# Performance work log

Hardware: AMD Instinct MI355X
Metric: run time of the kernel (lower is better)

## Reference

```python
import jax, jax.numpy as jnp
import numpy as np

N_NODES = 20000
N_EDGES = 320000
N_GRAPHS = 64
IN_FEAT = 64
HIDDEN = 256
GRID = 4
NUM_LAYERS = 4  # -> 3 Fourier message-passing layers
NEG_SLOPE = 0.01  # nn.LeakyReLU default


def setup_inputs() -> dict:
    key = jax.random.key(0)
    ks = jax.random.split(key, 8)
    h = jax.random.normal(ks[0], (N_NODES, IN_FEAT), dtype=jnp.float32)
    src = jax.random.randint(ks[1], (N_EDGES,), 0, N_NODES, dtype=jnp.int32)
    dst = jax.random.randint(ks[2], (N_EDGES,), 0, N_NODES, dtype=jnp.int32)
    graph_ids = jnp.sort(jax.random.randint(ks[3], (N_NODES,), 0, N_GRAPHS, dtype=jnp.int32))
    # KAN_polynomial(in_feat, hidden, degree=grid_feat), init randn/(sqrt(in)*sqrt(deg))
    W_line = jax.random.normal(ks[4], (HIDDEN, IN_FEAT, GRID + 1), dtype=jnp.float32) / (
        np.sqrt(IN_FEAT) * np.sqrt(GRID))
    # 3 NaiveFourierKANLayer coeffs [2, out, in, grid]
    fourier_coeffs = jax.random.normal(ks[5], (NUM_LAYERS - 1, 2, HIDDEN, HIDDEN, GRID),
                                       dtype=jnp.float32) / (np.sqrt(HIDDEN) * np.sqrt(GRID))
    # Readout KAN_polynomial(hidden, 1, degree=1, addbias=True)
    W_out = jax.random.normal(ks[6], (1, HIDDEN, 2), dtype=jnp.float32) / np.sqrt(HIDDEN)
    b_out = jnp.zeros((1, 1), dtype=jnp.float32)
    return {"h": h, "src": src, "dst": dst, "graph_ids": graph_ids,
            "W_line": W_line, "fourier_coeffs": fourier_coeffs,
            "W_out": W_out, "b_out": b_out}


def kan_polynomial(x, coeffs, bias=None):
    # x: [b, in], coeffs: [out, in, deg+1]
    deg = coeffs.shape[-1] - 1
    powers = jnp.stack([x ** i for i in range(deg + 1)], axis=-1)  # [b, in, deg+1]
    y = jnp.einsum('bid,oid->bo', powers, coeffs)
    if bias is not None:
        y = y + bias
    return y


def fourier_kan(x, coeffs):
    # x: [N, in], coeffs: [2, out, in, grid]
    grid = coeffs.shape[-1]
    k = jnp.arange(1, grid + 1, dtype=x.dtype)  # [grid]
    ang = x[:, :, None] * k  # [N, in, grid]
    y = jnp.einsum('nig,oig->no', jnp.cos(ang), coeffs[0])
    y = y + jnp.einsum('nig,oig->no', jnp.sin(ang), coeffs[1])
    return y


def reference(h, src, dst, graph_ids, W_line, fourier_coeffs, W_out, b_out):
    # kan_line
    h = kan_polynomial(h, W_line)  # [N, hidden]
    # message-passing Fourier KAN layers with residual + leaky_relu
    for l in range(NUM_LAYERS - 1):
        agg = jax.ops.segment_sum(h[src], dst, num_segments=N_NODES)  # copy_u + sum
        m = fourier_kan(agg, fourier_coeffs[l])
        h = jax.nn.leaky_relu(m + h, negative_slope=NEG_SLOPE)
    # avg pooling per graph
    sums = jax.ops.segment_sum(h, graph_ids, num_segments=N_GRAPHS)  # [G, hidden]
    counts = jax.ops.segment_sum(jnp.ones((N_NODES,), dtype=h.dtype), graph_ids,
                                 num_segments=N_GRAPHS)
    y = sums / jnp.maximum(counts, 1.0)[:, None]
    # Readout: KAN_polynomial(hidden, 1, degree=1) + sigmoid
    out = jax.nn.sigmoid(kan_polynomial(y, W_out, b_out))  # [G, 1]
    return out
```

## Files before the change

kernel.cpp:

```cpp
#include <hip/hip_runtime.h>
#include <math.h>

#define N_NODES   20000
#define N_PAD2    20096
#define N_EDGES   320000
#define N_GRAPHS  64
#define IN_FEAT   64
#define HIDDEN    256
#define GRID_F    4
#define NLAYERS   3
#define NEG_SLOPE 0.01f

#define KF 2048
#define KL4 256
#define NB_SCAN 79
#define NRG  157
#define NBLK (NRG * 4)
#define NLBLK 1256

typedef _Float16 f16x8 __attribute__((ext_vector_type(8)));
typedef _Float16 f16x2 __attribute__((ext_vector_type(2)));
typedef float    f32x4 __attribute__((ext_vector_type(4)));

__global__ void transpose_fourier_f16(const float* __restrict__ fc, _Float16* __restrict__ Bt) {
    int idx = blockIdx.x * 256 + threadIdx.x;
    int kk  = idx & 2047;
    int rest = idx >> 11;
    int o = rest & 255;
    int l = rest >> 8;
    int i = kk >> 3, f = kk & 7, g = f >> 1, t = f & 1;
    Bt[idx] = (_Float16)fc[(((size_t)(l * 2 + t) * HIDDEN + o) * HIDDEN + i) * GRID_F + g];
}

__global__ void transpose_line4(const float* __restrict__ wl, _Float16* __restrict__ Wth,
                                _Float16* __restrict__ Wtl) {
    int idx = blockIdx.x * 256 + threadIdx.x;
    int o = idx >> 8, kk = idx & 255;
    int i = kk >> 2, d = (kk & 3) + 1;
    float wv = wl[(o * IN_FEAT + i) * 5 + d];
    _Float16 h = (_Float16)wv;
    Wth[idx] = h;
    Wtl[idx] = (_Float16)(wv - (float)h);
}

__global__ void line_bias(const float* __restrict__ wl, float* __restrict__ biasv) {
    int o = threadIdx.x;
    float s = 0.f;
    for (int i = 0; i < IN_FEAT; ++i) s += wl[(o * IN_FEAT + i) * 5];
    biasv[o] = s;
}

__global__ void count_deg(const int* __restrict__ dst, int* __restrict__ counts) {
    int e = blockIdx.x * 256 + threadIdx.x;
    if (e < N_EDGES) atomicAdd(&counts[dst[e]], 1);
}

__global__ void block_sums(const int* __restrict__ counts, int* __restrict__ bsum) {
    int i = blockIdx.x * 256 + threadIdx.x;
    int v = (i < N_NODES) ? counts[i] : 0;
    #pragma unroll
    for (int o = 32; o > 0; o >>= 1) v += __shfl_down(v, o, 64);
    __shared__ int ws[4];
    if ((threadIdx.x & 63) == 0) ws[threadIdx.x >> 6] = v;
    __syncthreads();
    if (threadIdx.x == 0) bsum[blockIdx.x] = ws[0] + ws[1] + ws[2] + ws[3];
}

__global__ void scan_mid(const int* __restrict__ bsum, int* __restrict__ bofs,
                         int* __restrict__ row_start) {
    __shared__ int buf[128];
    int t = threadIdx.x;
    int v = (t < NB_SCAN) ? bsum[t] : 0;
    buf[t] = v;
    __syncthreads();
    for (int d = 1; d < 128; d <<= 1) {
        int x = (t >= d) ? buf[t - d] : 0;
        __syncthreads();
        buf[t] += x;
        __syncthreads();
    }
    if (t < NB_SCAN) bofs[t] = buf[t] - v;
    if (t == NB_SCAN - 1) row_start[N_NODES] = buf[t];
}

__global__ void scan_blocks(const int* __restrict__ counts, const int* __restrict__ bofs,
                            int* __restrict__ row_start) {
    int i = blockIdx.x * 256 + threadIdx.x;
    int val = (i < N_NODES) ? counts[i] : 0;
    int lane = threadIdx.x & 63, wid = threadIdx.x >> 6;
    int v = val;
    #pragma unroll
    for (int d = 1; d < 64; d <<= 1) {
        int t = __shfl_up(v, d, 64);
        if (lane >= d) v += t;
    }
    __shared__ int ws[4];
    if (lane == 63) ws[wid] = v;
    __syncthreads();
    int wofs = 0;
    for (int j = 0; j < wid; ++j) wofs += ws[j];
    if (i < N_NODES) row_start[i] = bofs[blockIdx.x] + wofs + v - val;
}

__global__ void fill_csr(const int* __restrict__ src, const int* __restrict__ dst,
                         const int* __restrict__ row_start, int* __restrict__ cursor,
                         int* __restrict__ ssrc) {
    int e = blockIdx.x * 256 + threadIdx.x;
    if (e < N_EDGES) {
        int d = dst[e];
        int pos = row_start[d] + atomicAdd(&cursor[d], 1);
        ssrc[pos] = src[e];
    }
}

__global__ __launch_bounds__(256)
void aggregate(const float* __restrict__ h, const int* __restrict__ row_start,
               const int* __restrict__ ssrc, unsigned* __restrict__ cs) {
    const int node = blockIdx.x * 4 + (threadIdx.x >> 6);
    const int lane = threadIdx.x & 63;
    const int b = row_start[node], e = row_start[node + 1];
    f32x4 a0 = {0.f, 0.f, 0.f, 0.f}, a1 = {0.f, 0.f, 0.f, 0.f};
    f32x4 a2 = {0.f, 0.f, 0.f, 0.f}, a3 = {0.f, 0.f, 0.f, 0.f};
    int j = b;
    for (; j + 3 < e; j += 4) {
        int s0 = ssrc[j], s1 = ssrc[j + 1], s2 = ssrc[j + 2], s3 = ssrc[j + 3];
        a0 += *(const f32x4*)&h[(size_t)s0 * HIDDEN + lane * 4];
        a1 += *(const f32x4*)&h[(size_t)s1 * HIDDEN + lane * 4];
        a2 += *(const f32x4*)&h[(size_t)s2 * HIDDEN + lane * 4];
        a3 += *(const f32x4*)&h[(size_t)s3 * HIDDEN + lane * 4];
    }
    for (; j < e; ++j) {
        int s0 = ssrc[j];
        a0 += *(const f32x4*)&h[(size_t)s0 * HIDDEN + lane * 4];
    }
    f32x4 v = (a0 + a1) + (a2 + a3);
    unsigned csv[4];
    #pragma unroll
    for (int k = 0; k < 4; ++k) {
        float r = v[k] * 0.15915494309189535f;
        r -= floorf(r);
        _Float16 ch = (_Float16)__builtin_amdgcn_cosf(r);
        _Float16 sh = (_Float16)__builtin_amdgcn_sinf(r);
        union { f16x2 z; unsigned u; } p;
        p.z = (f16x2){ch, sh};
        csv[k] = p.u;
    }
    *(uint4*)&cs[(size_t)node * HIDDEN + lane * 4] = make_uint4(csv[0], csv[1], csv[2], csv[3]);
}

__device__ __forceinline__ void makepow(float xa, float xb, f16x8& hi, f16x8& lo) {
    float p0 = xa, p1 = xa * xa;
    float p2 = p1 * xa, p3 = p1 * p1;
    float q0 = xb, q1 = xb * xb;
    float q2 = q1 * xb, q3 = q1 * q1;
    float pp[8] = {p0, p1, p2, p3, q0, q1, q2, q3};
    #pragma unroll
    for (int j = 0; j < 8; ++j) {
        _Float16 h = (_Float16)pp[j];
        hi[j] = h;
        lo[j] = (_Float16)(pp[j] - (float)h);
    }
}

__global__ __launch_bounds__(256)
void kan_line_mfma(const float* __restrict__ x, const _Float16* __restrict__ Wth,
                   const _Float16* __restrict__ Wtl, const float* __restrict__ biasv,
                   float* __restrict__ out) {
    __shared__ float    As[64][64];
    __shared__ _Float16 Bsh[64][136];
    __shared__ _Float16 Bsl[64][136];

    const int t = threadIdx.x;
    const int w = t >> 6, l = t & 63, ln = l & 15, quad = l >> 4;
    const int wr = w >> 1, wc = w & 1;

    const int g   = blockIdx.x;
    const int bid = (g & 7) * 157 + (g >> 3);
    const int Mbase = (bid >> 2) * 64;
    const int col0  = (bid & 3) * 64;

    #pragma unroll
    for (int r = 0; r < 4; ++r) {
        int idx = r * 256 + t;
        int row = idx >> 4, p = idx & 15;
        int grow = Mbase + row;
        if (grow > N_NODES - 1) grow = N_NODES - 1;
        f32x4 v = *(const f32x4*)&x[(size_t)grow * IN_FEAT + p * 4];
        *(f32x4*)&As[row][(p * 4) ^ ((row & 7) << 2)] = v;
    }
    const _Float16* WthB = Wth + (size_t)col0 * KL4;
    const _Float16* WtlB = Wtl + (size_t)col0 * KL4;
    #pragma unroll
    for (int r = 0; r < 4; ++r) {
        int idx = r * 256 + t;
        int c = idx >> 4, p = idx & 15;
        *(f16x8*)&Bsh[c][p * 8] = *(const f16x8*)&WthB[(size_t)c * KL4 + p * 8];
        *(f16x8*)&Bsl[c][p * 8] = *(const f16x8*)&WtlB[(size_t)c * KL4 + p * 8];
    }
    f16x8 pbh[4], pbl[4];
    #pragma unroll
    for (int r = 0; r < 4; ++r) {
        int idx = r * 256 + t;
        int c = idx >> 4, p = idx & 15;
        pbh[r] = *(const f16x8*)&WthB[(size_t)c * KL4 + 128 + p * 8];
        pbl[r] = *(const f16x8*)&WtlB[(size_t)c * KL4 + 128 + p * 8];
    }
    __syncthreads();

    f32x4 acc[2][2];
    #pragma unroll
    for (int rt = 0; rt < 2; ++rt)
        #pragma unroll
        for (int ct = 0; ct < 2; ++ct)
            acc[rt][ct] = (f32x4){0.f, 0.f, 0.f, 0.f};

    const int lr0 = wr * 32 + ln;
    const int xsw = (lr0 & 7) << 2;

    #pragma unroll
    for (int half = 0; half < 2; ++half) {
        #pragma unroll
        for (int kcl = 0; kcl < 4; ++kcl) {
            const int kc = half * 4 + kcl;
            const int f0 = kc * 8 + quad * 2;
            float x00 = As[lr0     ][f0 ^ xsw];
            float x01 = As[lr0     ][(f0 + 1) ^ xsw];
            float x10 = As[lr0 + 16][f0 ^ xsw];
            float x11 = As[lr0 + 16][(f0 + 1) ^ xsw];
            f16x8 ah0, al0, ah1, al1;
            makepow(x00, x01, ah0, al0);
            makepow(x10, x11, ah1, al1);
            #pragma unroll
            for (int ct = 0; ct < 2; ++ct) {
                const int bc = wc * 32 + ct * 16 + ln;
                f16x8 bh = *(const f16x8*)&Bsh[bc][kcl * 32 + quad * 8];
                f16x8 bl = *(const f16x8*)&Bsl[bc][kcl * 32 + quad * 8];
                acc[0][ct] = __builtin_amdgcn_mfma_f32_16x16x32_f16(ah0, bh, acc[0][ct], 0, 0, 0);
                acc[0][ct] = __builtin_amdgcn_mfma_f32_16x16x32_f16(al0, bh, acc[0][ct], 0, 0, 0);
                acc[0][ct] = __builtin_amdgcn_mfma_f32_16x16x32_f16(ah0, bl, acc[0][ct], 0, 0, 0);
                acc[1][ct] = __builtin_amdgcn_mfma_f32_16x16x32_f16(ah1, bh, acc[1][ct], 0, 0, 0);
                acc[1][ct] = __builtin_amdgcn_mfma_f32_16x16x32_f16(al1, bh, acc[1][ct], 0, 0, 0);
                acc[1][ct] = __builtin_amdgcn_mfma_f32_16x16x32_f16(ah1, bl, acc[1][ct], 0, 0, 0);
            }
        }
        if (half == 0) {
            __syncthreads();
            #pragma unroll
            for (int r = 0; r < 4; ++r) {
                int idx = r * 256 + t;
                int c = idx >> 4, p = idx & 15;
                *(f16x8*)&Bsh[c][p * 8] = pbh[r];
                *(f16x8*)&Bsl[c][p * 8] = pbl[r];
            }
            __syncthreads();
        }
    }

    #pragma unroll
    for (int rt = 0; rt < 2; ++rt) {
        const int row0 = Mbase + wr * 32 + rt * 16 + quad * 4;
        #pragma unroll
        for (int ct = 0; ct < 2; ++ct) {
            const int col = col0 + wc * 32 + ct * 16 + ln;
            const float bv = biasv[col];
            #pragma unroll
            for (int r = 0; r < 4; ++r) {
                const int row = row0 + r;
                if (row < N_NODES)
                    out[(size_t)row * HIDDEN + col] = acc[rt][ct][r] + bv;
            }
        }
    }
}

__device__ __forceinline__ f16x8 expand4(unsigned csu) {
    union { unsigned u; f16x2 z; } w; w.u = csu;
    f16x2 z1 = w.z;
    f16x2 cc = {z1[0], z1[0]};
    f16x2 ms = {(_Float16)(-z1[1]), z1[1]};
    f16x2 z2 = z1 * cc + (f16x2){z1[1], z1[0]} * ms;
    f16x2 z3 = z2 * cc + (f16x2){z2[1], z2[0]} * ms;
    f16x2 z4 = z3 * cc + (f16x2){z3[1], z3[0]} * ms;
    union { f16x8 v; f16x2 p[4]; } u;
    u.p[0] = z1; u.p[1] = z2; u.p[2] = z3; u.p[3] = z4;
    return u.v;
}

__global__ __launch_bounds__(256)
void fourier_mfma(const unsigned* __restrict__ cs, float* hio,
                  const _Float16* __restrict__ Bt) {
    __shared__ _Float16 Bs[2][64][140];
    __shared__ unsigned As[2][128][17];

    const int t    = threadIdx.x;
    const int w    = t >> 6;
    const int l    = t & 63;
    const int ln   = l & 15;
    const int quad = l >> 4;

    const int g   = blockIdx.x;
    const int xcd = g & 7, ii = g >> 3;
    const int bid = (xcd < 4 ? xcd * 79 : 316 + (xcd - 4) * 78) + ii;
    const int Mbase = (bid >> 2) * 128;
    const int col0  = (bid & 3) * 64;

    const int sc = t >> 4, sp = t & 15;
    const int sr = t >> 2, sq = t & 3;
    const _Float16* bg0 = Bt + (size_t)(col0 + sc) * KF + sp * 8;
    const _Float16* bg1 = bg0 + (size_t)16 * KF;
    const _Float16* bg2 = bg0 + (size_t)32 * KF;
    const _Float16* bg3 = bg0 + (size_t)48 * KF;
    const unsigned* ag0 = cs + (size_t)(Mbase + sr) * HIDDEN + sq * 4;
    const unsigned* ag1 = ag0 + (size_t)64 * HIDDEN;

    f32x4 acc[2][4];
    #pragma unroll
    for (int rt = 0; rt < 2; ++rt)
        #pragma unroll
        for (int ct = 0; ct < 4; ++ct)
            acc[rt][ct] = (f32x4){0.f, 0.f, 0.f, 0.f};

    f16x8 sb0, sb1, sb2, sb3;
    uint4 sa0, sa1;

    sb0 = *(const f16x8*)(bg0);
    sb1 = *(const f16x8*)(bg1);
    sb2 = *(const f16x8*)(bg2);
    sb3 = *(const f16x8*)(bg3);
    sa0 = *(const uint4*)(ag0);
    sa1 = *(const uint4*)(ag1);
    *(f16x8*)&Bs[0][sc     ][sp * 8] = sb0;
    *(f16x8*)&Bs[0][sc + 16][sp * 8] = sb1;
    *(f16x8*)&Bs[0][sc + 32][sp * 8] = sb2;
    *(f16x8*)&Bs[0][sc + 48][sp * 8] = sb3;
    As[0][sr     ][sq * 4 + 0] = sa0.x;
    As[0][sr     ][sq * 4 + 1] = sa0.y;
    As[0][sr     ][sq * 4 + 2] = sa0.z;
    As[0][sr     ][sq * 4 + 3] = sa0.w;
    As[0][sr + 64][sq * 4 + 0] = sa1.x;
    As[0][sr + 64][sq * 4 + 1] = sa1.y;
    As[0][sr + 64][sq * 4 + 2] = sa1.z;
    As[0][sr + 64][sq * 4 + 3] = sa1.w;
    __syncthreads();

    const int lr0 = w * 32 + ln;

    for (int kg = 0; kg < 16; ++kg) {
        const int b = kg & 1;
        if (kg < 15) {
            sb0 = *(const f16x8*)(bg0 + (kg + 1) * 128);
            sb1 = *(const f16x8*)(bg1 + (kg + 1) * 128);
            sb2 = *(const f16x8*)(bg2 + (kg + 1) * 128);
            sb3 = *(const f16x8*)(bg3 + (kg + 1) * 128);
            sa0 = *(const uint4*)(ag0 + (kg + 1) * 16);
            sa1 = *(const uint4*)(ag1 + (kg + 1) * 16);
        }
        #pragma unroll
        for (int kc = 0; kc < 4; ++kc) {
            unsigned cv0 = As[b][lr0     ][kc * 4 + quad];
            unsigned cv1 = As[b][lr0 + 16][kc * 4 + quad];
            f16x8 b0 = *(const f16x8*)&Bs[b][ln     ][kc * 32 + quad * 8];
            f16x8 b1 = *(const f16x8*)&Bs[b][ln + 16][kc * 32 + quad * 8];
            f16x8 b2 = *(const f16x8*)&Bs[b][ln + 32][kc * 32 + quad * 8];
            f16x8 b3 = *(const f16x8*)&Bs[b][ln + 48][kc * 32 + quad * 8];
            f16x8 a0 = expand4(cv0);
            f16x8 a1 = expand4(cv1);
            acc[0][0] = __builtin_amdgcn_mfma_f32_16x16x32_f16(a0, b0, acc[0][0], 0, 0, 0);
            acc[0][1] = __builtin_amdgcn_mfma_f32_16x16x32_f16(a0, b1, acc[0][1], 0, 0, 0);
            acc[0][2] = __builtin_amdgcn_mfma_f32_16x16x32_f16(a0, b2, acc[0][2], 0, 0, 0);
            acc[0][3] = __builtin_amdgcn_mfma_f32_16x16x32_f16(a0, b3, acc[0][3], 0, 0, 0);
            acc[1][0] = __builtin_amdgcn_mfma_f32_16x16x32_f16(a1, b0, acc[1][0], 0, 0, 0);
            acc[1][1] = __builtin_amdgcn_mfma_f32_16x16x32_f16(a1, b1, acc[1][1], 0, 0, 0);
            acc[1][2] = __builtin_amdgcn_mfma_f32_16x16x32_f16(a1, b2, acc[1][2], 0, 0, 0);
            acc[1][3] = __builtin_amdgcn_mfma_f32_16x16x32_f16(a1, b3, acc[1][3], 0, 0, 0);
        }
        if (kg < 15) {
            const int nb = b ^ 1;
            *(f16x8*)&Bs[nb][sc     ][sp * 8] = sb0;
            *(f16x8*)&Bs[nb][sc + 16][sp * 8] = sb1;
            *(f16x8*)&Bs[nb][sc + 32][sp * 8] = sb2;
            *(f16x8*)&Bs[nb][sc + 48][sp * 8] = sb3;
            As[nb][sr     ][sq * 4 + 0] = sa0.x;
            As[nb][sr     ][sq * 4 + 1] = sa0.y;
            As[nb][sr     ][sq * 4 + 2] = sa0.z;
            As[nb][sr     ][sq * 4 + 3] = sa0.w;
            As[nb][sr + 64][sq * 4 + 0] = sa1.x;
            As[nb][sr + 64][sq * 4 + 1] = sa1.y;
            As[nb][sr + 64][sq * 4 + 2] = sa1.z;
            As[nb][sr + 64][sq * 4 + 3] = sa1.w;
        }
        __syncthreads();
    }

    #pragma unroll
    for (int rt = 0; rt < 2; ++rt) {
        const int row0 = Mbase + w * 32 + rt * 16 + quad * 4;
        #pragma unroll
        for (int ct = 0; ct < 4; ++ct) {
            const int col = col0 + ct * 16 + ln;
            #pragma unroll
            for (int r = 0; r < 4; ++r) {
                const int row = row0 + r;
                if (row < N_NODES) {
                    float v = acc[rt][ct][r] + hio[(size_t)row * HIDDEN + col];
                    v = v > 0.f ? v : NEG_SLOPE * v;
                    hio[(size_t)row * HIDDEN + col] = v;
                }
            }
        }
    }
}

__global__ void graph_bounds(const int* __restrict__ gid, int* __restrict__ gstart) {
    int g = threadIdx.x;
    if (g < N_GRAPHS) {
        int lo = 0, hi = N_NODES;
        while (lo < hi) { int mid = (lo + hi) >> 1; if (gid[mid] < g) lo = mid + 1; else hi = mid; }
        gstart[g] = lo;
    } else if (g == N_GRAPHS) {
        gstart[g] = N_NODES;
    }
}

__global__ __launch_bounds__(256)
void pool_seg(const float* __restrict__ h, const int* __restrict__ gid,
              float* __restrict__ pooled) {
    const int c = threadIdx.x;
    const int s = blockIdx.x * 128;
    const int e = min(s + 128, N_NODES);
    float acc = 0.f;
    int g = gid[s];
    for (int n = s; n < e; ++n) {
        int gn = gid[n];
        if (gn != g) {
            atomicAdd(&pooled[g * HIDDEN + c], acc);
            acc = 0.f;
            g = gn;
        }
        acc += h[(size_t)n * HIDDEN + c];
    }
    atomicAdd(&pooled[g * HIDDEN + c], acc);
}

__global__ void readout(const float* __restrict__ pooled, const int* __restrict__ gstart,
                        const float* __restrict__ wout, const float* __restrict__ bout,
                        float* __restrict__ out) {
    int g = blockIdx.x, t = threadIdx.x;
    float cnt = fmaxf((float)(gstart[g + 1] - gstart[g]), 1.f);
    float y = pooled[g * HIDDEN + t] / cnt;
    float term = wout[t * 2 + 0] + wout[t * 2 + 1] * y;
    #pragma unroll
    for (int o = 32; o > 0; o >>= 1) term += __shfl_down(term, o, 64);
    __shared__ float wsum[4];
    if ((t & 63) == 0) wsum[t >> 6] = term;
    __syncthreads();
    if (t == 0) {
        float s = wsum[0] + wsum[1] + wsum[2] + wsum[3] + bout[0];
        out[g] = 1.f / (1.f + expf(-s));
    }
}

extern "C" void kernel_launch(void* const* d_in, const int* in_sizes, int n_in,
                              void* d_out, int out_size, void* d_ws, size_t ws_size,
                              hipStream_t stream) {
    const float* h_in  = (const float*)d_in[0];
    const int*   src   = (const int*)d_in[1];
    const int*   dst   = (const int*)d_in[2];
    const int*   gid   = (const int*)d_in[3];
    const float* wline = (const float*)d_in[4];
    const float* fcoef = (const float*)d_in[5];
    const float* wout  = (const float*)d_in[6];
    const float* bout  = (const float*)d_in[7];
    float* out = (float*)d_out;

    char* ws = (char*)d_ws;
    size_t off = 0;
    auto alloc = [&](size_t bytes) {
        size_t o = off;
        off += (bytes + 255) & ~size_t(255);
        return o;
    };
    float*     hbuf      = (float*)(ws + alloc((size_t)N_PAD2 * HIDDEN * 4));
    unsigned*  csbuf     = (unsigned*)(ws + alloc((size_t)N_PAD2 * HIDDEN * 4));
    _Float16*  BtF16     = (_Float16*)(ws + alloc((size_t)NLAYERS * KF * HIDDEN * 2));
    _Float16*  Wth       = (_Float16*)(ws + alloc((size_t)HIDDEN * KL4 * 2));
    _Float16*  Wtl       = (_Float16*)(ws + alloc((size_t)HIDDEN * KL4 * 2));
    float*     biasv     = (float*)(ws + alloc((size_t)HIDDEN * 4));
    int*       row_start = (int*)(ws + alloc((size_t)(N_NODES + 1) * 4));
    int*       counts    = (int*)(ws + alloc((size_t)N_NODES * 4));
    int*       cursor    = (int*)(ws + alloc((size_t)N_NODES * 4));
    int*       ssrc      = (int*)(ws + alloc((size_t)N_EDGES * 4));
    int*       bsum      = (int*)(ws + alloc((size_t)128 * 4));
    int*       bofs      = (int*)(ws + alloc((size_t)128 * 4));
    int*       gstart    = (int*)(ws + alloc((size_t)(N_GRAPHS + 1) * 4));
    float*     pooled    = (float*)(ws + alloc((size_t)N_GRAPHS * HIDDEN * 4));

    hipMemsetAsync(counts, 0, (size_t)N_NODES * 4, stream);
    hipMemsetAsync(cursor, 0, (size_t)N_NODES * 4, stream);
    hipMemsetAsync(pooled, 0, (size_t)N_GRAPHS * HIDDEN * 4, stream);
    hipMemsetAsync(csbuf + (size_t)N_NODES * HIDDEN, 0,
                   (size_t)(N_PAD2 - N_NODES) * HIDDEN * 4, stream);

    transpose_fourier_f16<<<6144, 256, 0, stream>>>(fcoef, BtF16);
    transpose_line4<<<256, 256, 0, stream>>>(wline, Wth, Wtl);
    line_bias<<<1, 256, 0, stream>>>(wline, biasv);
    count_deg<<<(N_EDGES + 255) / 256, 256, 0, stream>>>(dst, counts);
    block_sums<<<NB_SCAN, 256, 0, stream>>>(counts, bsum);
    scan_mid<<<1, 128, 0, stream>>>(bsum, bofs, row_start);
    scan_blocks<<<NB_SCAN, 256, 0, stream>>>(counts, bofs, row_start);
    fill_csr<<<(N_EDGES + 255) / 256, 256, 0, stream>>>(src, dst, row_start, cursor, ssrc);
    graph_bounds<<<1, 128, 0, stream>>>(gid, gstart);

    kan_line_mfma<<<NLBLK, 256, 0, stream>>>(h_in, Wth, Wtl, biasv, hbuf);

    for (int l = 0; l < NLAYERS; ++l) {
        aggregate<<<N_NODES / 4, 256, 0, stream>>>(hbuf, row_start, ssrc, csbuf);
        fourier_mfma<<<NBLK, 256, 0, stream>>>(csbuf, hbuf,
                                               BtF16 + (size_t)l * KF * HIDDEN);
    }

    pool_seg<<<(N_NODES + 127) / 128, 256, 0, stream>>>(hbuf, gid, pooled);
    readout<<<N_GRAPHS, 256, 0, stream>>>(pooled, gstart, wout, bout, out);
}
```

Measured before the change: 440.3 us.

## Aggregate 16-bit fixed-point phases instead of fp32 features in gather

Producer kernels now also store each feature's phase (x/2π mod 1) as a 16-bit fixed-point value. The aggregate kernel sums these phases with wrapping integer adds instead of gathering fp32 rows. Because sin and cos are periodic, the sum taken mod 1 gives the same angle as the fp32 sum, while the gather reads half the bytes. In exchange every producer writes an extra 2-byte store per element, and phase quantisation adds some angle error.

Measured after the change: 395.0 us, median of 2. -10.3%, faster.

```diff
diff --git a/kernel.cpp b/kernel.cpp
--- a/kernel.cpp
+++ b/kernel.cpp
@@ -21,6 +21,13 @@
 typedef _Float16 f16x8 __attribute__((ext_vector_type(8)));
 typedef _Float16 f16x2 __attribute__((ext_vector_type(2)));
 typedef float    f32x4 __attribute__((ext_vector_type(4)));
+typedef unsigned short u16x4 __attribute__((ext_vector_type(4)));
+
+__device__ __forceinline__ unsigned short phase16(float v) {
+    float r = v * 0.15915494309189535f;
+    r -= floorf(r);
+    return (unsigned short)((unsigned)(r * 65536.f + 0.5f) & 0xFFFFu);
+}
 
 __global__ void transpose_fourier_f16(const float* __restrict__ fc, _Float16* __restrict__ Bt) {
     int idx = blockIdx.x * 256 + threadIdx.x;
@@ -114,31 +121,29 @@
 }
 
 __global__ __launch_bounds__(256)
-void aggregate(const float* __restrict__ h, const int* __restrict__ row_start,
+void aggregate(const unsigned short* __restrict__ hq, const int* __restrict__ row_start,
                const int* __restrict__ ssrc, unsigned* __restrict__ cs) {
     const int node = blockIdx.x * 4 + (threadIdx.x >> 6);
     const int lane = threadIdx.x & 63;
     const int b = row_start[node], e = row_start[node + 1];
-    f32x4 a0 = {0.f, 0.f, 0.f, 0.f}, a1 = {0.f, 0.f, 0.f, 0.f};
-    f32x4 a2 = {0.f, 0.f, 0.f, 0.f}, a3 = {0.f, 0.f, 0.f, 0.f};
+    u16x4 a0 = {0, 0, 0, 0}, a1 = {0, 0, 0, 0}, a2 = {0, 0, 0, 0}, a3 = {0, 0, 0, 0};
     int j = b;
     for (; j + 3 < e; j += 4) {
         int s0 = ssrc[j], s1 = ssrc[j + 1], s2 = ssrc[j + 2], s3 = ssrc[j + 3];
-        a0 += *(const f32x4*)&h[(size_t)s0 * HIDDEN + lane * 4];
-        a1 += *(const f32x4*)&h[(size_t)s1 * HIDDEN + lane * 4];
-        a2 += *(const f32x4*)&h[(size_t)s2 * HIDDEN + lane * 4];
-        a3 += *(const f32x4*)&h[(size_t)s3 * HIDDEN + lane * 4];
+        a0 += *(const u16x4*)&hq[(size_t)s0 * HIDDEN + lane * 4];
+        a1 += *(const u16x4*)&hq[(size_t)s1 * HIDDEN + lane * 4];
+        a2 += *(const u16x4*)&hq[(size_t)s2 * HIDDEN + lane * 4];
+        a3 += *(const u16x4*)&hq[(size_t)s3 * HIDDEN + lane * 4];
     }
     for (; j < e; ++j) {
         int s0 = ssrc[j];
-        a0 += *(const f32x4*)&h[(size_t)s0 * HIDDEN + lane * 4];
-    }
-    f32x4 v = (a0 + a1) + (a2 + a3);
+        a0 += *(const u16x4*)&hq[(size_t)s0 * HIDDEN + lane * 4];
+    }
+    u16x4 s = (a0 + a1) + (a2 + a3);
     unsigned csv[4];
     #pragma unroll
     for (int k = 0; k < 4; ++k) {
-        float r = v[k] * 0.15915494309189535f;
-        r -= floorf(r);
+        float r = (float)s[k] * (1.f / 65536.f);
         _Float16 ch = (_Float16)__builtin_amdgcn_cosf(r);
         _Float16 sh = (_Float16)__builtin_amdgcn_sinf(r);
         union { f16x2 z; unsigned u; } p;
@@ -165,7 +170,7 @@
 __global__ __launch_bounds__(256)
 void kan_line_mfma(const float* __restrict__ x, const _Float16* __restrict__ Wth,
                    const _Float16* __restrict__ Wtl, const float* __restrict__ biasv,
-                   float* __restrict__ out) {
+                   float* __restrict__ out, unsigned short* __restrict__ hqo) {
     __shared__ float    As[64][64];
     __shared__ _Float16 Bsh[64][136];
     __shared__ _Float16 Bsl[64][136];
@@ -266,8 +271,11 @@
             #pragma unroll
             for (int r = 0; r < 4; ++r) {
                 const int row = row0 + r;
-                if (row < N_NODES)
-                    out[(size_t)row * HIDDEN + col] = acc[rt][ct][r] + bv;
+                if (row < N_NODES) {
+                    float vv = acc[rt][ct][r] + bv;
+                    out[(size_t)row * HIDDEN + col] = vv;
+                    hqo[(size_t)row * HIDDEN + col] = phase16(vv);
+                }
             }
         }
     }
@@ -288,7 +296,7 @@
 
 __global__ __launch_bounds__(256)
 void fourier_mfma(const unsigned* __restrict__ cs, float* hio,
-                  const _Float16* __restrict__ Bt) {
+                  const _Float16* __restrict__ Bt, unsigned short* __restrict__ hqo) {
     __shared__ _Float16 Bs[2][64][140];
     __shared__ unsigned As[2][128][17];
 
@@ -405,6 +413,7 @@
                     float v = acc[rt][ct][r] + hio[(size_t)row * HIDDEN + col];
                     v = v > 0.f ? v : NEG_SLOPE * v;
                     hio[(size_t)row * HIDDEN + col] = v;
+                    hqo[(size_t)row * HIDDEN + col] = phase16(v);
                 }
             }
         }
@@ -480,20 +489,21 @@
         off += (bytes + 255) & ~size_t(255);
         return o;
     };
-    float*     hbuf      = (float*)(ws + alloc((size_t)N_PAD2 * HIDDEN * 4));
-    unsigned*  csbuf     = (unsigned*)(ws + alloc((size_t)N_PAD2 * HIDDEN * 4));
-    _Float16*  BtF16     = (_Float16*)(ws + alloc((size_t)NLAYERS * KF * HIDDEN * 2));
-    _Float16*  Wth       = (_Float16*)(ws + alloc((size_t)HIDDEN * KL4 * 2));
-    _Float16*  Wtl       = (_Float16*)(ws + alloc((size_t)HIDDEN * KL4 * 2));
-    float*     biasv     = (float*)(ws + alloc((size_t)HIDDEN * 4));
-    int*       row_start = (int*)(ws + alloc((size_t)(N_NODES + 1) * 4));
-    int*       counts    = (int*)(ws + alloc((size_t)N_NODES * 4));
-    int*       cursor    = (int*)(ws + alloc((size_t)N_NODES * 4));
-    int*       ssrc      = (int*)(ws + alloc((size_t)N_EDGES * 4));
-    int*       bsum      = (int*)(ws + alloc((size_t)128 * 4));
-    int*       bofs      = (int*)(ws + alloc((size_t)128 * 4));
-    int*       gstart    = (int*)(ws + alloc((size_t)(N_GRAPHS + 1) * 4));
-    float*     pooled    = (float*)(ws + alloc((size_t)N_GRAPHS * HIDDEN * 4));
+    float*          hbuf      = (float*)(ws + alloc((size_t)N_PAD2 * HIDDEN * 4));
+    unsigned short* hqbuf     = (unsigned short*)(ws + alloc((size_t)N_PAD2 * HIDDEN * 2));
+    unsigned*       csbuf     = (unsigned*)(ws + alloc((size_t)N_PAD2 * HIDDEN * 4));
+    _Float16*       BtF16     = (_Float16*)(ws + alloc((size_t)NLAYERS * KF * HIDDEN * 2));
+    _Float16*       Wth       = (_Float16*)(ws + alloc((size_t)HIDDEN * KL4 * 2));
+    _Float16*       Wtl       = (_Float16*)(ws + alloc((size_t)HIDDEN * KL4 * 2));
+    float*          biasv     = (float*)(ws + alloc((size_t)HIDDEN * 4));
+    int*            row_start = (int*)(ws + alloc((size_t)(N_NODES + 1) * 4));
+    int*            counts    = (int*)(ws + alloc((size_t)N_NODES * 4));
+    int*            cursor    = (int*)(ws + alloc((size_t)N_NODES * 4));
+    int*            ssrc      = (int*)(ws + alloc((size_t)N_EDGES * 4));
+    int*            bsum      = (int*)(ws + alloc((size_t)128 * 4));
+    int*            bofs      = (int*)(ws + alloc((size_t)128 * 4));
+    int*            gstart    = (int*)(ws + alloc((size_t)(N_GRAPHS + 1) * 4));
+    float*          pooled    = (float*)(ws + alloc((size_t)N_GRAPHS * HIDDEN * 4));
 
     hipMemsetAsync(counts, 0, (size_t)N_NODES * 4, stream);
     hipMemsetAsync(cursor, 0, (size_t)N_NODES * 4, stream);
@@ -511,12 +521,12 @@
     fill_csr<<<(N_EDGES + 255) / 256, 256, 0, stream>>>(src, dst, row_start, cursor, ssrc);
     graph_bounds<<<1, 128, 0, stream>>>(gid, gstart);
 
-    kan_line_mfma<<<NLBLK, 256, 0, stream>>>(h_in, Wth, Wtl, biasv, hbuf);
+    kan_line_mfma<<<NLBLK, 256, 0, stream>>>(h_in, Wth, Wtl, biasv, hbuf, hqbuf);
 
     for (int l = 0; l < NLAYERS; ++l) {
-        aggregate<<<N_NODES / 4, 256, 0, stream>>>(hbuf, row_start, ssrc, csbuf);
+        aggregate<<<N_NODES / 4, 256, 0, stream>>>(hqbuf, row_start, ssrc, csbuf);
         fourier_mfma<<<NBLK, 256, 0, stream>>>(csbuf, hbuf,
-                                               BtF16 + (size_t)l * KF * HIDDEN);
+                                               BtF16 + (size_t)l * KF * HIDDEN, hqbuf);
     }
 
     pool_seg<<<(N_NODES + 127) / 128, 256, 0, stream>>>(hbuf, gid, pooled);
```
